# Kernel tuning notes

Hardware: AMD Instinct MI355X
Metric: run time of the kernel (lower is better)

Reference implementation:

```python
import jax, jax.numpy as jnp
import numpy as np

SQRT_2_OVER_PI = float(np.sqrt(2.0 / np.pi))

def gelu(x):
    return 0.5 * x * (1.0 + jnp.tanh(SQRT_2_OVER_PI * (x + 0.044715 * x ** 3)))

def layer_norm(x, w, b, eps=1e-5):
    mean = jnp.mean(x, axis=-1, keepdims=True)
    var = jnp.var(x, axis=-1, keepdims=True)
    return (x - mean) / jnp.sqrt(var + eps) * w + b

B, S, D, H = 4, 2048, 768, 12
HD = D // H

def setup_inputs() -> dict:
    key = jax.random.key(0)
    ks = jax.random.split(key, 13)
    sc = lambda fan_in: 1.0 / np.sqrt(fan_in)
    return {
        "x": jax.random.normal(ks[0], (B, S, D), jnp.float32),
        "ln1_w": jnp.ones((D,), jnp.float32),
        "ln1_b": jnp.zeros((D,), jnp.float32),
        "w_attn": jax.random.normal(ks[1], (D, 3 * D), jnp.float32) * sc(D),
        "b_attn": jax.random.normal(ks[2], (3 * D,), jnp.float32) * 0.02,
        "w_proj": jax.random.normal(ks[3], (D, D), jnp.float32) * sc(D),
        "b_proj": jax.random.normal(ks[4], (D,), jnp.float32) * 0.02,
        "ln2_w": jnp.ones((D,), jnp.float32),
        "ln2_b": jnp.zeros((D,), jnp.float32),
        "w_fc": jax.random.normal(ks[5], (D, 4 * D), jnp.float32) * sc(D),
        "b_fc": jax.random.normal(ks[6], (4 * D,), jnp.float32) * 0.02,
        "w_fc_proj": jax.random.normal(ks[7], (4 * D, D), jnp.float32) * sc(4 * D),
        "b_fc_proj": jax.random.normal(ks[8], (D,), jnp.float32) * 0.02,
    }

def reference(x, ln1_w, ln1_b, w_attn, b_attn, w_proj, b_proj,
              ln2_w, ln2_b, w_fc, b_fc, w_fc_proj, b_fc_proj):
    batch, seq, dim = x.shape
    # --- causal self-attention on ln_1(x) ---
    h = layer_norm(x, ln1_w, ln1_b)
    qkv = h @ w_attn + b_attn                       # [B,S,3D]
    q, k, v = jnp.split(qkv, 3, axis=-1)
    qh = q.reshape(batch, seq, H, HD).transpose(0, 2, 1, 3)  # [B,H,S,hd]
    kh = k.reshape(batch, seq, H, HD).transpose(0, 2, 1, 3)
    vh = v.reshape(batch, seq, H, HD).transpose(0, 2, 1, 3)
    scores = jnp.einsum('bhqd,bhkd->bhqk', qh, kh) / np.sqrt(HD)  # [B,H,S,S]
    causal = jnp.tril(jnp.ones((seq, seq), bool))
    scores = jnp.where(causal, scores, -jnp.inf)
    probs = jax.nn.softmax(scores, axis=-1)
    attn = jnp.einsum('bhqk,bhkd->bhqd', probs, vh)  # [B,H,S,hd]
    attn = attn.transpose(0, 2, 1, 3).reshape(batch, seq, dim)
    x = x + attn @ w_proj + b_proj
    # --- MLP on ln_2(x) ---
    h = layer_norm(x, ln2_w, ln2_b)
    h = gelu(h @ w_fc + b_fc)
    x = x + h @ w_fc_proj + b_fc_proj
    return x
```

## Files before the change

### kernel.cpp

```cpp
#include <hip/hip_runtime.h>

typedef __bf16 bf16x8 __attribute__((ext_vector_type(8)));
typedef float f32x4 __attribute__((ext_vector_type(4)));
typedef unsigned short u16;
typedef u16 u16x8 __attribute__((ext_vector_type(8)));
typedef u16 u16x4 __attribute__((ext_vector_type(4)));

#define DEVI static __device__ __forceinline__

DEVI u16 f2bf(float f) {
  unsigned u = __float_as_uint(f);
  u += 0x7FFFu + ((u >> 16) & 1u);
  return (u16)(u >> 16);
}
DEVI float bf2f(u16 u) { return __uint_as_float(((unsigned)u) << 16); }

DEVI void gload_lds16(const void* g, void* l) {
  __builtin_amdgcn_global_load_lds((const __attribute__((address_space(1))) void*)g,
                                   (__attribute__((address_space(3))) void*)l, 16, 0, 0);
}

__global__ __launch_bounds__(256) void k_transpose_w(const float* __restrict__ in,
                                                     u16* __restrict__ out, int R, int C) {
  __shared__ float tile[64][65];
  const int t = threadIdx.x;
  const int c0 = blockIdx.x * 64, r0 = blockIdx.y * 64;
#pragma unroll
  for (int i = 0; i < 4; ++i) {
    int id = t + i * 256;
    int r = id >> 4, c4 = (id & 15) * 4;
    f32x4 v = *(const f32x4*)(in + (size_t)(r0 + r) * C + c0 + c4);
#pragma unroll
    for (int j = 0; j < 4; ++j) tile[r][c4 + j] = v[j];
  }
  __syncthreads();
  const int oc = t >> 2;
  const int rr = (t & 3) * 16;
  u16x8 lo, hi;
#pragma unroll
  for (int j = 0; j < 8; ++j) lo[j] = f2bf(tile[rr + j][oc]);
#pragma unroll
  for (int j = 0; j < 8; ++j) hi[j] = f2bf(tile[rr + 8 + j][oc]);
  u16* dst = out + (size_t)(c0 + oc) * R + r0 + rr;
  *(u16x8*)dst = lo;
  *(u16x8*)(dst + 8) = hi;
}

__global__ __launch_bounds__(256) void k_transpose_v(const u16* __restrict__ qkv,
                                                     u16* __restrict__ vt) {
  __shared__ u16 tile[64][72];
  const int t = threadIdx.x;
  const int bh = blockIdx.y;
  const int b = bh / 12, h = bh % 12;
  const int s0 = blockIdx.x * 64;
  const u16* src = qkv + (size_t)b * 2048 * 2304 + 1536 + h * 64;
#pragma unroll
  for (int i = 0; i < 2; ++i) {
    int id = t + i * 256;
    int r = id >> 3, c8 = (id & 7) * 8;
    *(u16x8*)&tile[r][c8] = *(const u16x8*)(src + (size_t)(s0 + r) * 2304 + c8);
  }
  __syncthreads();
  const int od = t >> 2;
  const int rr = (t & 3) * 16;
  u16x8 lo, hi;
#pragma unroll
  for (int j = 0; j < 8; ++j) lo[j] = tile[rr + j][od];
#pragma unroll
  for (int j = 0; j < 8; ++j) hi[j] = tile[rr + 8 + j][od];
  u16* dst = vt + ((size_t)bh * 64 + od) * 2048 + s0 + rr;
  *(u16x8*)dst = lo;
  *(u16x8*)(dst + 8) = hi;
}

__global__ __launch_bounds__(192) void k_layernorm(const float* __restrict__ x,
                                                   const float* __restrict__ w,
                                                   const float* __restrict__ bvec,
                                                   u16* __restrict__ out) {
  const int row = blockIdx.x, t = threadIdx.x;
  const float* xr = x + (size_t)row * 768;
  f32x4 v = *(const f32x4*)(xr + t * 4);
  float s = v[0] + v[1] + v[2] + v[3];
  float sq = v[0] * v[0] + v[1] * v[1] + v[2] * v[2] + v[3] * v[3];
#pragma unroll
  for (int m = 1; m < 64; m <<= 1) { s += __shfl_xor(s, m); sq += __shfl_xor(sq, m); }
  __shared__ float red[2][3];
  const int wv = t >> 6;
  if ((t & 63) == 0) { red[0][wv] = s; red[1][wv] = sq; }
  __syncthreads();
  s = red[0][0] + red[0][1] + red[0][2];
  sq = red[1][0] + red[1][1] + red[1][2];
  const float mean = s * (1.0f / 768.0f);
  const float var = sq * (1.0f / 768.0f) - mean * mean;
  const float rstd = rsqrtf(var + 1e-5f);
  f32x4 wv4 = *(const f32x4*)(w + t * 4);
  f32x4 bv4 = *(const f32x4*)(bvec + t * 4);
  u16x4 o;
#pragma unroll
  for (int j = 0; j < 4; ++j) o[j] = f2bf((v[j] - mean) * rstd * wv4[j] + bv4[j]);
  *(u16x4*)(out + (size_t)row * 768 + t * 4) = o;
}

#define EPI_QKV 0
#define EPI_RESID 1
#define EPI_GELU 2

template <int EPI>
__global__ __launch_bounds__(256) void k_gemm(const u16* __restrict__ A,
                                              const u16* __restrict__ BT,
                                              const float* __restrict__ bias,
                                              const float* __restrict__ resid,
                                              void* __restrict__ outp,
                                              int M, int N, int K) {
  __shared__ u16 As[128 * 32];
  __shared__ u16 Bs[128 * 32];
  const int t = threadIdx.x;
  const int lane = t & 63, w = t >> 6;
  const int l15 = lane & 15, l4 = lane >> 4;
  const int wr = w >> 1, wc = w & 1;
  const int m0 = blockIdx.y * 128, n0 = blockIdx.x * 128;

  f32x4 acc[4][4] = {};

  for (int kt = 0; kt < K; kt += 32) {
#pragma unroll
    for (int i = 0; i < 2; ++i) {
      int c = w * 128 + i * 64 + lane;
      int m = c >> 2, k16 = (c & 3) * 8;
      gload_lds16(A + (size_t)(m0 + m) * K + kt + k16, As + c * 8);
    }
#pragma unroll
    for (int i = 0; i < 2; ++i) {
      int c = w * 128 + i * 64 + lane;
      int n = c >> 2, k16 = (c & 3) * 8;
      gload_lds16(BT + (size_t)(n0 + n) * K + kt + k16, Bs + c * 8);
    }
    __syncthreads();
    bf16x8 af[4], bfr[4];
#pragma unroll
    for (int f = 0; f < 4; ++f)
      af[f] = *(const bf16x8*)(As + (wr * 64 + f * 16 + l15) * 32 + l4 * 8);
#pragma unroll
    for (int f = 0; f < 4; ++f)
      bfr[f] = *(const bf16x8*)(Bs + (wc * 64 + f * 16 + l15) * 32 + l4 * 8);
#pragma unroll
    for (int fi = 0; fi < 4; ++fi)
#pragma unroll
      for (int fj = 0; fj < 4; ++fj)
        acc[fi][fj] = __builtin_amdgcn_mfma_f32_16x16x32_bf16(af[fi], bfr[fj], acc[fi][fj], 0, 0, 0);
    __syncthreads();
  }

#pragma unroll
  for (int fi = 0; fi < 4; ++fi) {
    const int mbase = m0 + wr * 64 + fi * 16 + l4 * 4;
#pragma unroll
    for (int fj = 0; fj < 4; ++fj) {
      const int n = n0 + wc * 64 + fj * 16 + l15;
      const float bn = bias[n];
#pragma unroll
      for (int r = 0; r < 4; ++r) {
        const size_t idx = (size_t)(mbase + r) * N + n;
        float val = acc[fi][fj][r] + bn;
        if constexpr (EPI == EPI_QKV) {
          ((u16*)outp)[idx] = f2bf(val);
        } else if constexpr (EPI == EPI_RESID) {
          ((float*)outp)[idx] = val + resid[idx];
        } else {
          float z2 = 1.5957691216057308f * (val + 0.044715f * val * val * val);
          float g = val / (1.0f + exp2f(-1.4426950408889634f * z2));
          ((u16*)outp)[idx] = f2bf(g);
        }
      }
    }
  }
}

__global__ __launch_bounds__(512) void k_attn(const u16* __restrict__ qkv,
                                              const u16* __restrict__ vt,
                                              u16* __restrict__ out) {
  __shared__ u16 Ks[2][64 * 64];
  __shared__ u16 Vs[2][64 * 64];
  __shared__ u16 Ps[8][16 * 72];
  const int t = threadIdx.x, lane = t & 63, w = t >> 6;
  const int l15 = lane & 15, l4 = lane >> 4;
  const int l44 = l4 * 4;
  const int qb = (int)gridDim.x - 1 - (int)blockIdx.x;
  const int h = blockIdx.y, b = blockIdx.z;
  const int q0 = qb * 128;
  const int qw = q0 + w * 16;
  const u16* qbase = qkv + (size_t)b * 2048 * 2304 + h * 64;
  const u16* kbase = qbase + 768;
  const u16* vtb = vt + ((size_t)(b * 12 + h) * 64) * 2048;

  const int sr = t >> 3;
  const int scx = (t & 7) ^ (sr & 7);
  const size_t kgo = (size_t)sr * 2304 + scx * 8;
  const size_t vgo = (size_t)sr * 2048 + scx * 8;

  const int rx0 = ((l4 ^ (l15 & 7)) * 8);
  const int rx1 = (((4 + l4) ^ (l15 & 7)) * 8);

  const int qrow = qw + l15;
  bf16x8 qf0, qf1;
  {
    const float PRE = 0.18033688011112042f;
    u16x8 r0 = *(const u16x8*)(qbase + (size_t)qrow * 2304 + l4 * 8);
    u16x8 r1 = *(const u16x8*)(qbase + (size_t)qrow * 2304 + 32 + l4 * 8);
    u16x8 s0, s1;
#pragma unroll
    for (int j = 0; j < 8; ++j) { s0[j] = f2bf(bf2f(r0[j]) * PRE); s1[j] = f2bf(bf2f(r1[j]) * PRE); }
    qf0 = *(bf16x8*)&s0;
    qf1 = *(bf16x8*)&s1;
  }

  float m_run = -1e30f, l_run = 0.f;
  f32x4 o_acc[4] = {};
  u16* pw = &Ps[w][0];
  const int qq = qw + l15;

  const int ntiles = 2 * qb + 2;

  gload_lds16(kbase + kgo, (char*)&Ks[0][0] + t * 16);
  gload_lds16(vtb + vgo, (char*)&Vs[0][0] + t * 16);

  for (int kt = 0; kt < ntiles; ++kt) {
    __syncthreads();
    if (kt + 1 < ntiles) {
      const int nb = (kt + 1) & 1;
      gload_lds16(kbase + (size_t)(kt + 1) * 64 * 2304 + kgo, (char*)&Ks[nb][0] + t * 16);
      gload_lds16(vtb + (size_t)(kt + 1) * 64 + vgo, (char*)&Vs[nb][0] + t * 16);
    }
    const int kv0 = kt * 64;
    if (kv0 <= qw + 15) {
      const u16* kb = &Ks[kt & 1][0];
      const u16* vb = &Vs[kt & 1][0];
      f32x4 sa[4] = {};
      __builtin_amdgcn_s_setprio(1);
#pragma unroll
      for (int c = 0; c < 4; ++c) {
        bf16x8 kf0 = *(const bf16x8*)(kb + (c * 16 + l15) * 64 + rx0);
        bf16x8 kf1 = *(const bf16x8*)(kb + (c * 16 + l15) * 64 + rx1);
        sa[c] = __builtin_amdgcn_mfma_f32_16x16x32_bf16(kf0, qf0, sa[c], 0, 0, 0);
        sa[c] = __builtin_amdgcn_mfma_f32_16x16x32_bf16(kf1, qf1, sa[c], 0, 0, 0);
      }
      __builtin_amdgcn_s_setprio(0);

      if (kv0 + 63 > qw) {
#pragma unroll
        for (int c = 0; c < 4; ++c)
#pragma unroll
          for (int r = 0; r < 4; ++r)
            if (kv0 + c * 16 + l44 + r > qq) sa[c][r] = -1e30f;
      }

      float pm = fmaxf(fmaxf(sa[0][0], sa[0][1]), fmaxf(sa[0][2], sa[0][3]));
#pragma unroll
      for (int c = 1; c < 4; ++c)
        pm = fmaxf(pm, fmaxf(fmaxf(sa[c][0], sa[c][1]), fmaxf(sa[c][2], sa[c][3])));
      pm = fmaxf(pm, __shfl_xor(pm, 16));
      pm = fmaxf(pm, __shfl_xor(pm, 32));

      if (__any(pm > m_run + 8.0f)) {
        float mn = fmaxf(m_run, pm);
        float scq = exp2f(m_run - mn);
        m_run = mn;
        l_run *= scq;
#pragma unroll
        for (int r = 0; r < 4; ++r) {
          float s = __shfl(scq, l44 + r);
#pragma unroll
          for (int cd = 0; cd < 4; ++cd) o_acc[cd][r] *= s;
        }
      }

      float ls = 0.f;
      u16x4 pk[4];
#pragma unroll
      for (int c = 0; c < 4; ++c)
#pragma unroll
        for (int r = 0; r < 4; ++r) {
          float p = exp2f(sa[c][r] - m_run);
          ls += p;
          pk[c][r] = f2bf(p);
        }
      ls += __shfl_xor(ls, 16);
      ls += __shfl_xor(ls, 32);
      l_run += ls;

#pragma unroll
      for (int c = 0; c < 4; ++c)
        *(u16x4*)(pw + l15 * 72 + c * 16 + l44) = pk[c];

      bf16x8 pa0 = *(const bf16x8*)(pw + l15 * 72 + l4 * 8);
      bf16x8 pa1 = *(const bf16x8*)(pw + l15 * 72 + 32 + l4 * 8);

      __builtin_amdgcn_s_setprio(1);
#pragma unroll
      for (int cd = 0; cd < 4; ++cd) {
        bf16x8 vf0 = *(const bf16x8*)(vb + (cd * 16 + l15) * 64 + rx0);
        bf16x8 vf1 = *(const bf16x8*)(vb + (cd * 16 + l15) * 64 + rx1);
        o_acc[cd] = __builtin_amdgcn_mfma_f32_16x16x32_bf16(pa0, vf0, o_acc[cd], 0, 0, 0);
        o_acc[cd] = __builtin_amdgcn_mfma_f32_16x16x32_bf16(pa1, vf1, o_acc[cd], 0, 0, 0);
      }
      __builtin_amdgcn_s_setprio(0);
    }
  }

  float lr[4];
#pragma unroll
  for (int r = 0; r < 4; ++r) lr[r] = 1.0f / __shfl(l_run, l44 + r);
#pragma unroll
  for (int cd = 0; cd < 4; ++cd)
#pragma unroll
    for (int r = 0; r < 4; ++r) {
      int qr = qw + l44 + r;
      out[((size_t)(b * 2048) + qr) * 768 + h * 64 + cd * 16 + l15] = f2bf(o_acc[cd][r] * lr[r]);
    }
}

extern "C" void kernel_launch(void* const* d_in, const int* in_sizes, int n_in,
                              void* d_out, int out_size, void* d_ws, size_t ws_size,
                              hipStream_t stream) {
  (void)in_sizes; (void)n_in; (void)out_size; (void)ws_size;
  const float* x      = (const float*)d_in[0];
  const float* ln1_w  = (const float*)d_in[1];
  const float* ln1_b  = (const float*)d_in[2];
  const float* w_attn = (const float*)d_in[3];
  const float* b_attn = (const float*)d_in[4];
  const float* w_proj = (const float*)d_in[5];
  const float* b_proj = (const float*)d_in[6];
  const float* ln2_w  = (const float*)d_in[7];
  const float* ln2_b  = (const float*)d_in[8];
  const float* w_fc   = (const float*)d_in[9];
  const float* b_fc   = (const float*)d_in[10];
  const float* w_fcp  = (const float*)d_in[11];
  const float* b_fcp  = (const float*)d_in[12];
  float* out = (float*)d_out;

  char* ws = (char*)d_ws;
  u16*   wt_attn = (u16*)(ws + 0);
  u16*   wt_proj = (u16*)(ws + 3538944);
  u16*   wt_fc   = (u16*)(ws + 4718592);
  u16*   wt_fcp  = (u16*)(ws + 9437184);
  u16*   h_ln    = (u16*)(ws + 14155776);
  u16*   qkv     = (u16*)(ws + 26738688);
  u16*   vtb     = (u16*)(ws + 64487424);
  u16*   h_gelu  = qkv;
  u16*   attn    = (u16*)(ws + 77070336);
  float* x2      = (float*)(ws + 89653248);

  k_transpose_w<<<dim3(36, 12), 256, 0, stream>>>(w_attn, wt_attn, 768, 2304);
  k_transpose_w<<<dim3(12, 12), 256, 0, stream>>>(w_proj, wt_proj, 768, 768);
  k_transpose_w<<<dim3(48, 12), 256, 0, stream>>>(w_fc, wt_fc, 768, 3072);
  k_transpose_w<<<dim3(12, 48), 256, 0, stream>>>(w_fcp, wt_fcp, 3072, 768);
  k_layernorm<<<8192, 192, 0, stream>>>(x, ln1_w, ln1_b, h_ln);
  k_gemm<EPI_QKV><<<dim3(18, 64), 256, 0, stream>>>(h_ln, wt_attn, b_attn, nullptr, qkv, 8192, 2304, 768);
  k_transpose_v<<<dim3(32, 48), 256, 0, stream>>>(qkv, vtb);
  k_attn<<<dim3(16, 12, 4), 512, 0, stream>>>(qkv, vtb, attn);
  k_gemm<EPI_RESID><<<dim3(6, 64), 256, 0, stream>>>(attn, wt_proj, b_proj, x, x2, 8192, 768, 768);
  k_layernorm<<<8192, 192, 0, stream>>>(x2, ln2_w, ln2_b, h_ln);
  k_gemm<EPI_GELU><<<dim3(24, 64), 256, 0, stream>>>(h_ln, wt_fc, b_fc, nullptr, h_gelu, 8192, 3072, 768);
  k_gemm<EPI_RESID><<<dim3(6, 64), 256, 0, stream>>>(h_gelu, wt_fcp, b_fcp, x2, out, 8192, 768, 3072);
}
```

Baseline: 472.5 us.

## Add double-buffered 256x256 GEMM kernel for QKV and FC projections

Adds a new GEMM kernel with 256x256 output tiles, 512 threads and a K-step of 64. A and B tiles are double-buffered in LDS and fetched with direct global-to-LDS loads, using an XOR-swizzled layout to avoid bank conflicts. Workgroup order is remapped into groups of eight, and MFMA phases are split by barriers and raised wave priority so the next tile's loads overlap compute. The kernel replaces the 128x128 single-buffered GEMM for the QKV and FC projections to raise operand reuse and hide memory latency. It uses 128 KB of LDS per block, which limits occupancy to one block per CU, and the QKV grid has only 288 blocks, which may leave the GPU partly underfilled.

Result: slower. 493.6 us (+4.5%).

```diff
diff --git a/kernel.cpp b/kernel.cpp
--- a/kernel.cpp
+++ b/kernel.cpp
@@ -19,6 +19,13 @@
   __builtin_amdgcn_global_load_lds((const __attribute__((address_space(1))) void*)g,
                                    (__attribute__((address_space(3))) void*)l, 16, 0, 0);
 }
+
+#define BARRIER()                                   \
+  do {                                              \
+    asm volatile("" ::: "memory");                  \
+    __builtin_amdgcn_s_barrier();                   \
+    asm volatile("" ::: "memory");                  \
+  } while (0)
 
 __global__ __launch_bounds__(256) void k_transpose_w(const float* __restrict__ in,
                                                      u16* __restrict__ out, int R, int C) {
@@ -104,6 +111,11 @@
 #define EPI_QKV 0
 #define EPI_RESID 1
 #define EPI_GELU 2
+
+DEVI float epi_gelu(float val) {
+  float z2 = 1.5957691216057308f * (val + 0.044715f * val * val * val);
+  return val / (1.0f + exp2f(-1.4426950408889634f * z2));
+}
 
 template <int EPI>
 __global__ __launch_bounds__(256) void k_gemm(const u16* __restrict__ A,
@@ -167,9 +179,158 @@
         } else if constexpr (EPI == EPI_RESID) {
           ((float*)outp)[idx] = val + resid[idx];
         } else {
-          float z2 = 1.5957691216057308f * (val + 0.044715f * val * val * val);
-          float g = val / (1.0f + exp2f(-1.4426950408889634f * z2));
-          ((u16*)outp)[idx] = f2bf(g);
+          ((u16*)outp)[idx] = f2bf(epi_gelu(val));
+        }
+      }
+    }
+  }
+}
+
+template <int EPI>
+__global__ __launch_bounds__(512, 2) void k_gemm256(const u16* __restrict__ A,
+                                                    const u16* __restrict__ BT,
+                                                    const float* __restrict__ bias,
+                                                    void* __restrict__ outp,
+                                                    int M, int N, int K) {
+  __shared__ u16 As[2][256 * 64];
+  __shared__ u16 Bs[2][256 * 64];
+  const int t = threadIdx.x, lane = t & 63, w = t >> 6;
+  const int l15 = lane & 15, l4 = lane >> 4;
+  const int wm = w >> 2, wn = w & 3;
+
+  const int gx = gridDim.x;
+  const int nwg = gx * gridDim.y;
+  const int lin = blockIdx.y * gx + blockIdx.x;
+  const int swz = (lin & 7) * (nwg >> 3) + (lin >> 3);
+  const int by = swz / gx, bx = swz - by * gx;
+  const int m0 = by * 256, n0 = bx * 256;
+
+  const int srow0 = t >> 3;
+  const int scoff = ((t & 7) ^ (srow0 & 7)) * 8;
+  const u16* srcA[4];
+  const u16* srcB[4];
+#pragma unroll
+  for (int g = 0; g < 4; ++g) {
+    srcA[g] = A + (size_t)(m0 + g * 64 + srow0) * K + scoff;
+    srcB[g] = BT + (size_t)(n0 + g * 64 + srow0) * K + scoff;
+  }
+
+  const int NT = K >> 6;
+  f32x4 acc[8][4] = {};
+  bf16x8 af[4][2], bf[4][2];
+
+#pragma unroll
+  for (int g = 0; g < 4; ++g) gload_lds16(srcA[g], (char*)&As[0][0] + (g * 512 + t) * 16);
+#pragma unroll
+  for (int g = 0; g < 4; ++g) gload_lds16(srcB[g], (char*)&Bs[0][0] + (g * 512 + t) * 16);
+  asm volatile("s_waitcnt vmcnt(0)" ::: "memory");
+  __builtin_amdgcn_s_barrier();
+  asm volatile("" ::: "memory");
+
+  for (int kt = 0; kt < NT; ++kt) {
+    const char* Ab = (const char*)&As[kt & 1][0];
+    const char* Bb = (const char*)&Bs[kt & 1][0];
+    char* An = (char*)&As[(kt + 1) & 1][0];
+    char* Bn = (char*)&Bs[(kt + 1) & 1][0];
+    const size_t ko = (size_t)((kt + 1 < NT) ? kt + 1 : kt) * 64;
+
+#pragma unroll
+    for (int g = 0; g < 4; ++g) gload_lds16(srcA[g] + ko, An + (g * 512 + t) * 16);
+#pragma unroll
+    for (int g = 0; g < 4; ++g) gload_lds16(srcB[g] + ko, Bn + (g * 512 + t) * 16);
+#pragma unroll
+    for (int f = 0; f < 4; ++f)
+#pragma unroll
+      for (int s = 0; s < 2; ++s) {
+        int row = wm * 128 + f * 16 + l15;
+        af[f][s] = *(const bf16x8*)(Ab + row * 128 + ((s * 4 + l4) ^ (row & 7)) * 16);
+      }
+#pragma unroll
+    for (int g = 0; g < 2; ++g)
+#pragma unroll
+      for (int s = 0; s < 2; ++s) {
+        int row = wn * 64 + g * 16 + l15;
+        bf[g][s] = *(const bf16x8*)(Bb + row * 128 + ((s * 4 + l4) ^ (row & 7)) * 16);
+      }
+    BARRIER();
+    __builtin_amdgcn_s_setprio(1);
+#pragma unroll
+    for (int f = 0; f < 4; ++f)
+#pragma unroll
+      for (int g = 0; g < 2; ++g)
+#pragma unroll
+        for (int s = 0; s < 2; ++s)
+          acc[f][g] = __builtin_amdgcn_mfma_f32_16x16x32_bf16(af[f][s], bf[g][s], acc[f][g], 0, 0, 0);
+    __builtin_amdgcn_s_setprio(0);
+    BARRIER();
+
+#pragma unroll
+    for (int g = 2; g < 4; ++g)
+#pragma unroll
+      for (int s = 0; s < 2; ++s) {
+        int row = wn * 64 + g * 16 + l15;
+        bf[g][s] = *(const bf16x8*)(Bb + row * 128 + ((s * 4 + l4) ^ (row & 7)) * 16);
+      }
+    BARRIER();
+    __builtin_amdgcn_s_setprio(1);
+#pragma unroll
+    for (int f = 0; f < 4; ++f)
+#pragma unroll
+      for (int g = 2; g < 4; ++g)
+#pragma unroll
+        for (int s = 0; s < 2; ++s)
+          acc[f][g] = __builtin_amdgcn_mfma_f32_16x16x32_bf16(af[f][s], bf[g][s], acc[f][g], 0, 0, 0);
+    __builtin_amdgcn_s_setprio(0);
+    BARRIER();
+
+#pragma unroll
+    for (int f = 0; f < 4; ++f)
+#pragma unroll
+      for (int s = 0; s < 2; ++s) {
+        int row = wm * 128 + 64 + f * 16 + l15;
+        af[f][s] = *(const bf16x8*)(Ab + row * 128 + ((s * 4 + l4) ^ (row & 7)) * 16);
+      }
+    BARRIER();
+    __builtin_amdgcn_s_setprio(1);
+#pragma unroll
+    for (int f = 0; f < 4; ++f)
+#pragma unroll
+      for (int g = 0; g < 2; ++g)
+#pragma unroll
+        for (int s = 0; s < 2; ++s)
+          acc[4 + f][g] = __builtin_amdgcn_mfma_f32_16x16x32_bf16(af[f][s], bf[g][s], acc[4 + f][g], 0, 0, 0);
+    __builtin_amdgcn_s_setprio(0);
+    BARRIER();
+
+    __builtin_amdgcn_s_setprio(1);
+#pragma unroll
+    for (int f = 0; f < 4; ++f)
+#pragma unroll
+      for (int g = 2; g < 4; ++g)
+#pragma unroll
+        for (int s = 0; s < 2; ++s)
+          acc[4 + f][g] = __builtin_amdgcn_mfma_f32_16x16x32_bf16(af[f][s], bf[g][s], acc[4 + f][g], 0, 0, 0);
+    __builtin_amdgcn_s_setprio(0);
+    asm volatile("s_waitcnt vmcnt(0)" ::: "memory");
+    __builtin_amdgcn_s_barrier();
+    asm volatile("" ::: "memory");
+  }
+
+#pragma unroll
+  for (int f = 0; f < 8; ++f) {
+    const int mbase = m0 + wm * 128 + f * 16 + l4 * 4;
+#pragma unroll
+    for (int g = 0; g < 4; ++g) {
+      const int n = n0 + wn * 64 + g * 16 + l15;
+      const float bn = bias[n];
+#pragma unroll
+      for (int r = 0; r < 4; ++r) {
+        const size_t idx = (size_t)(mbase + r) * N + n;
+        float val = acc[f][g][r] + bn;
+        if constexpr (EPI == EPI_QKV) {
+          ((u16*)outp)[idx] = f2bf(val);
+        } else {
+          ((u16*)outp)[idx] = f2bf(epi_gelu(val));
         }
       }
     }
@@ -355,11 +516,11 @@
   k_transpose_w<<<dim3(48, 12), 256, 0, stream>>>(w_fc, wt_fc, 768, 3072);
   k_transpose_w<<<dim3(12, 48), 256, 0, stream>>>(w_fcp, wt_fcp, 3072, 768);
   k_layernorm<<<8192, 192, 0, stream>>>(x, ln1_w, ln1_b, h_ln);
-  k_gemm<EPI_QKV><<<dim3(18, 64), 256, 0, stream>>>(h_ln, wt_attn, b_attn, nullptr, qkv, 8192, 2304, 768);
+  k_gemm256<EPI_QKV><<<dim3(9, 32), 512, 0, stream>>>(h_ln, wt_attn, b_attn, qkv, 8192, 2304, 768);
   k_transpose_v<<<dim3(32, 48), 256, 0, stream>>>(qkv, vtb);
   k_attn<<<dim3(16, 12, 4), 512, 0, stream>>>(qkv, vtb, attn);
   k_gemm<EPI_RESID><<<dim3(6, 64), 256, 0, stream>>>(attn, wt_proj, b_proj, x, x2, 8192, 768, 768);
   k_layernorm<<<8192, 192, 0, stream>>>(x2, ln2_w, ln2_b, h_ln);
-  k_gemm<EPI_GELU><<<dim3(24, 64), 256, 0, stream>>>(h_ln, wt_fc, b_fc, nullptr, h_gelu, 8192, 3072, 768);
+  k_gemm256<EPI_GELU><<<dim3(12, 32), 512, 0, stream>>>(h_ln, wt_fc, b_fc, h_gelu, 8192, 3072, 768);
   k_gemm<EPI_RESID><<<dim3(6, 64), 256, 0, stream>>>(h_gelu, wt_fcp, b_fcp, x2, out, 8192, 768, 3072);
 }
```
